# Kernel optimization log

Hardware: AMD Instinct MI355X
Metric: run time of the kernel (lower is better)

The kernel has to match this reference:

```python
import jax, jax.numpy as jnp
import numpy as np

B, N, F, P, HID, OUT = 4, 20000, 8, 12, 64, 1
E = 320000


def _glorot(k, shape):
    lim = float(np.sqrt(6.0 / (shape[0] + shape[1])))
    return jax.random.uniform(k, shape, jnp.float32, -lim, lim)


def setup_inputs() -> dict:
    key = jax.random.key(0)
    ks = jax.random.split(key, 20)
    inp = {
        "x": jax.random.normal(ks[0], (B, N, F, P), jnp.float32),
        "edge_index": jax.random.randint(ks[1], (2, E), 0, N, jnp.int64),
        "edge_attr": jax.random.uniform(ks[2], (E,), jnp.float32),
        # GCNConv weights (stored [in, out]) + biases for z, r, h gates
        "conv_z_w": _glorot(ks[3], (F, HID)), "conv_z_b": jnp.zeros((HID,), jnp.float32),
        "conv_r_w": _glorot(ks[4], (F, HID)), "conv_r_b": jnp.zeros((HID,), jnp.float32),
        "conv_h_w": _glorot(ks[5], (F, HID)), "conv_h_b": jnp.zeros((HID,), jnp.float32),
        # GRU linear layers on cat([conv_out, H]) -> HID (stored [in, out])
        "lin_z_w": _glorot(ks[6], (2 * HID, HID)), "lin_z_b": jnp.zeros((HID,), jnp.float32),
        "lin_r_w": _glorot(ks[7], (2 * HID, HID)), "lin_r_b": jnp.zeros((HID,), jnp.float32),
        "lin_h_w": _glorot(ks[8], (2 * HID, HID)), "lin_h_b": jnp.zeros((HID,), jnp.float32),
        # temporal attention logits over periods
        "attention": jax.random.uniform(ks[9], (P,), jnp.float32),
        # final linear: HID -> OUT*P
        "out_w": _glorot(ks[10], (HID, OUT * P)), "out_b": jnp.zeros((OUT * P,), jnp.float32),
    }
    return inp


def reference(x, edge_index, edge_attr,
              conv_z_w, conv_z_b, conv_r_w, conv_r_b, conv_h_w, conv_h_b,
              lin_z_w, lin_z_b, lin_r_w, lin_r_b, lin_h_w, lin_h_b,
              attention, out_w, out_b):
    Bb, Nn, Ff, Pp = x.shape
    Hh = conv_z_w.shape[1]

    # GCN normalization with self loops: A_hat = D^-1/2 (A + I) D^-1/2
    loop = jnp.arange(Nn)
    row = jnp.concatenate([edge_index[0], loop])
    col = jnp.concatenate([edge_index[1], loop])
    w = jnp.concatenate([edge_attr, jnp.ones((Nn,), x.dtype)])
    deg = jax.ops.segment_sum(w, col, num_segments=Nn)
    dinv = jnp.where(deg > 0, jax.lax.rsqrt(deg), 0.0)
    norm = dinv[row] * w * dinv[col]  # [E+N]

    def gcn(xt, W, b):
        # xt: [B, N, F] -> [B, N, H]
        xw = jnp.einsum('bnf,fh->bnh', xt, W)
        msg = xw[:, row, :] * norm[None, :, None]            # gather over source nodes
        agg = jax.vmap(lambda m: jax.ops.segment_sum(m, col, num_segments=Nn))(msg)
        return agg + b

    H0 = jnp.zeros((Bb, Nn, Hh), x.dtype)  # A3TGCN2 passes H=None each period -> zeros

    def tgcn_cell(xt):
        Z = jax.nn.sigmoid(jnp.concatenate([gcn(xt, conv_z_w, conv_z_b), H0], -1) @ lin_z_w + lin_z_b)
        R = jax.nn.sigmoid(jnp.concatenate([gcn(xt, conv_r_w, conv_r_b), H0], -1) @ lin_r_w + lin_r_b)
        Ht = jnp.tanh(jnp.concatenate([gcn(xt, conv_h_w, conv_h_b), H0 * R], -1) @ lin_h_w + lin_h_b)
        return Z * H0 + (1.0 - Z) * Ht

    probs = jax.nn.softmax(attention)
    xs = jnp.moveaxis(x, -1, 0)  # [P, B, N, F]

    def step(acc, inp):
        xt, p = inp
        return acc + p * tgcn_cell(xt), None

    h_accum, _ = jax.lax.scan(step, jnp.zeros((Bb, Nn, Hh), x.dtype), (xs, probs))

    h = jax.nn.relu(h_accum)
    out = h @ out_w + out_b                 # [B, N, OUT*P]
    return out.reshape(Bb, Nn, -1, Pp)      # [B, N, OUT, P]
```

## Files before the change

### kernel.cpp

```cpp
#include <hip/hip_runtime.h>

#define NN 20000
#define EE 320000
#define CAP 64
#define SVC 72
#define OVCAP 8192
#define EBLK 313

#define WZ_O 0
#define BZ_O 512
#define WH_O 576
#define BH_O 1088
#define OWT_O 1152
#define OB_O 1968
#define PR_O 1980
#define NCONST 1992

#define LOG2E 1.44269504088896340736f

__device__ __forceinline__ float b2f(unsigned short h) {
  union { unsigned int u; float f; } v; v.u = ((unsigned int)h) << 16; return v.f;
}
__device__ __forceinline__ unsigned short f2b(float f) {
  union { unsigned int u; float f; } v; v.f = f;
  unsigned int u = v.u;
  unsigned int r = (u + 0x7fffu + ((u >> 16) & 1u)) >> 16;
  return (unsigned short)r;
}
__device__ __forceinline__ float ldw(const void* p, int i, int isbf) {
  return isbf ? b2f(((const unsigned short*)p)[i]) : ((const float*)p)[i];
}
__device__ __forceinline__ void upk(unsigned int w, float& x0, float& x1) {
  union { unsigned int u; float f; } lo, hi;
  lo.u = w << 16; hi.u = w & 0xffff0000u;
  x0 = lo.f; x1 = hi.f;
}
__device__ __forceinline__ float degf(unsigned long long dc) {
  return (float)(unsigned int)dc * (1.0f / 1048576.0f);
}
__device__ __forceinline__ float ex2(float x) {
#if __has_builtin(__builtin_amdgcn_exp2f)
  return __builtin_amdgcn_exp2f(x);
#else
  return __exp2f(x);
#endif
}

struct __align__(4) U3 { unsigned int x, y, z; };

__global__ void __launch_bounds__(256) k_append(
    const void* __restrict__ ei, const void* __restrict__ ea,
    unsigned long long* __restrict__ degcnt,
    unsigned int* __restrict__ slab,
    int* __restrict__ ovf_cnt, int* __restrict__ ovf_dst,
    unsigned int* __restrict__ ovf_pack, float* __restrict__ consts,
    const void* czw, const void* czb, const void* chw, const void* chb,
    const void* lzw, const void* lzb, const void* lhw, const void* lhb,
    const void* att, const void* ow, const void* ob) {
  __shared__ int sfl[2];
  const int tid = threadIdx.x;
  if (tid < 64) {
    unsigned long long b1 = __ballot((((const unsigned int*)ea)[tid] >> 15) & 1u);
    unsigned long long b2 = __ballot(((const unsigned int*)ei)[2 * tid + 1] != 0u);
    if (tid == 0) {
      sfl[0] = (b1 == 0ull) ? 1 : 0;
      sfl[1] = (b2 == 0ull) ? 1 : 0;
    }
  }
  __syncthreads();
  const int isbf = sfl[0], is64 = sfl[1];

  if (blockIdx.x == EBLK) {
    for (int idx = tid; idx < 512; idx += 256) {
      int f = idx >> 6, k = idx & 63;
      float sz = 0.f, sh = 0.f;
      for (int h = 0; h < 64; ++h) {
        sz += ldw(czw, f * 64 + h, isbf) * ldw(lzw, h * 64 + k, isbf);
        sh += ldw(chw, f * 64 + h, isbf) * ldw(lhw, h * 64 + k, isbf);
      }
      consts[WZ_O + idx] = sz * LOG2E;
      consts[WH_O + idx] = sh * (2.0f * LOG2E);
    }
    for (int idx = tid; idx < 64; idx += 256) {
      float sz = ldw(lzb, idx, isbf), sh = ldw(lhb, idx, isbf);
      for (int h = 0; h < 64; ++h) {
        sz += ldw(czb, h, isbf) * ldw(lzw, h * 64 + idx, isbf);
        sh += ldw(chb, h, isbf) * ldw(lhw, h * 64 + idx, isbf);
      }
      consts[BZ_O + idx] = sz * LOG2E;
      consts[BH_O + idx] = sh * (2.0f * LOG2E);
    }
    for (int idx = tid; idx < 816; idx += 256) {
      int p = idx / 68, kk = idx % 68;
      consts[OWT_O + idx] = (kk < 64) ? ldw(ow, kk * 12 + p, isbf) : 0.f;
    }
    if (tid < 12) consts[OB_O + tid] = ldw(ob, tid, isbf);
    if (tid == 0) {
      float a[12]; float m = -1e30f;
      for (int p = 0; p < 12; ++p) { a[p] = ldw(att, p, isbf); m = fmaxf(m, a[p]); }
      float ssum = 0.f;
      for (int p = 0; p < 12; ++p) { a[p] = __expf(a[p] - m); ssum += a[p]; }
      for (int p = 0; p < 12; ++p) consts[PR_O + p] = a[p] / ssum;
    }
    return;
  }

  const int e0 = blockIdx.x * 1024 + tid;
#pragma unroll
  for (int u = 0; u < 4; ++u) {
    int e = e0 + 256 * u;
    if (e >= EE) continue;
    int r, c;
    if (is64) {
      r = (int)((const unsigned int*)ei)[2 * e];
      c = (int)((const unsigned int*)ei)[2 * (EE + e)];
    } else {
      r = ((const int*)ei)[e];
      c = ((const int*)ei)[EE + e];
    }
    unsigned short wb;
    float w;
    if (isbf) { wb = ((const unsigned short*)ea)[e]; w = b2f(wb); }
    else      { w = ((const float*)ea)[e]; wb = f2b(w); }
    unsigned long long pk = (1ull << 32) |
        (unsigned long long)(unsigned int)__float2int_rn(w * 1048576.0f);
    unsigned long long old = atomicAdd(&degcnt[c], pk);
    int pos = (int)(old >> 32);
    unsigned int packed = ((unsigned int)wb << 16) | (unsigned int)r;
    if (pos < CAP) {
      slab[c * CAP + pos] = packed;
    } else {
      int oi = atomicAdd(ovf_cnt, 1);
      if (oi < OVCAP) { ovf_dst[oi] = c; ovf_pack[oi] = packed; }
    }
  }
}

#define ACC6(u, v)                                           \
  { float x0, x1;                                            \
    upk((u).x, x0, x1); a[0] += (v) * x0; a[1] += (v) * x1;  \
    upk((u).y, x0, x1); a[2] += (v) * x0; a[3] += (v) * x1;  \
    upk((u).z, x0, x1); a[4] += (v) * x0; a[5] += (v) * x1; }

#define ACCF6(f0, f1, f2, v)                                                   \
  { a[0] += (v) * (f0).x; a[1] += (v) * (f0).y; a[2] += (v) * (f1).x;          \
    a[3] += (v) * (f1).y; a[4] += (v) * (f2).x; a[5] += (v) * (f2).y; }

__global__ void __launch_bounds__(256) k_node(
    const void* __restrict__ x, const void* __restrict__ ea,
    const unsigned long long* __restrict__ degcnt,
    const unsigned int* __restrict__ slab,
    const int* __restrict__ ovf_cnt, const int* __restrict__ ovf_dst,
    const unsigned int* __restrict__ ovf_pack,
    const float* __restrict__ consts,
    void* __restrict__ out) {
  __shared__ __align__(16) float sow[840];
  __shared__ __align__(16) int2  sv[4 * SVC];
  __shared__ __align__(16) float accT[4 * 384];
  __shared__ __align__(16) float hw[4 * 272];
  __shared__ int swcnt[4];
  __shared__ int sfl[1];

  const int tid  = threadIdx.x;
  const int w    = tid >> 6;
  const int lane = tid & 63;
  const int n    = blockIdx.x * 4 + w;

  if (tid < 64) {
    unsigned long long b1 = __ballot((((const unsigned int*)ea)[tid] >> 15) & 1u);
    if (tid == 0) sfl[0] = (b1 == 0ull) ? 1 : 0;
  }
  for (int i = tid; i < 840; i += 256) sow[i] = consts[OWT_O + i];
  float wz[8], wh[8];
#pragma unroll
  for (int f = 0; f < 8; ++f) {
    wz[f] = consts[WZ_O + f * 64 + lane];
    wh[f] = consts[WH_O + f * 64 + lane];
  }
  const float bz = consts[BZ_O + lane], bh = consts[BH_O + lane];
  __syncthreads();
  const int isbf = sfl[0];

  unsigned long long dcn = degcnt[n];
  int cnt = (int)(dcn >> 32);
  int base = cnt < CAP ? cnt : CAP;
  const float dn = rsqrtf(degf(dcn) + 1.0f);
  int2* svw = &sv[w * SVC];
  if (lane == 0) swcnt[w] = base;
  if (lane < base) {
    unsigned int pk = slab[n * CAP + lane];
    int s = (int)(pk & 0xffffu);
    float v = b2f((unsigned short)(pk >> 16)) * rsqrtf(degf(degcnt[s]) + 1.0f) * dn;
    svw[lane] = make_int2(s * 96, __float_as_int(v));
  }
  int m0 = base;
  {
    int ov = ovf_cnt[0];
    if (ov > 0) {
      if (ov > OVCAP) ov = OVCAP;
      for (int i = lane; i < ov; i += 64) {
        if (ovf_dst[i] == n) {
          int idx = atomicAdd(&swcnt[w], 1);
          if (idx < SVC - 1) {
            unsigned int pk = ovf_pack[i];
            int s = (int)(pk & 0xffffu);
            float v = b2f((unsigned short)(pk >> 16)) *
                      rsqrtf(degf(degcnt[s]) + 1.0f) * dn;
            svw[idx] = make_int2(s * 96, __float_as_int(v));
          }
        }
      }
      __builtin_amdgcn_wave_barrier();
      m0 = swcnt[w];
      if (m0 > SVC - 1) m0 = SVC - 1;
    }
  }
  if (lane == 0) svw[m0] = make_int2(n * 96, __float_as_int(dn * dn));
  const int m1 = m0 + 1;
  __builtin_amdgcn_wave_barrier();

  float a[6];
#pragma unroll
  for (int t = 0; t < 6; ++t) a[t] = 0.f;
  {
    const int i15 = lane & 15;
    const long xbase = (long)(lane >> 4) * (NN * 96) + 6 * i15;
    if (isbf) {
      const unsigned short* xr = (const unsigned short*)x + xbase;
      int j = 0;
      for (; j + 1 < m1; j += 2) {
        int2 e0 = svw[j], e1 = svw[j + 1];
        U3 u0 = *(const U3*)(xr + e0.x);
        U3 u1 = *(const U3*)(xr + e1.x);
        float v0 = __int_as_float(e0.y), v1 = __int_as_float(e1.y);
        ACC6(u0, v0); ACC6(u1, v1);
      }
      if (j < m1) {
        int2 e0 = svw[j];
        U3 u0 = *(const U3*)(xr + e0.x);
        float v0 = __int_as_float(e0.y);
        ACC6(u0, v0);
      }
    } else {
      const float* xf = (const float*)x + xbase;
      int j = 0;
      for (; j + 1 < m1; j += 2) {
        int2 e0 = svw[j], e1 = svw[j + 1];
        const float2* p0 = (const float2*)(xf + e0.x);
        const float2* p1 = (const float2*)(xf + e1.x);
        float2 u00 = p0[0], u01 = p0[1], u02 = p0[2];
        float2 u10 = p1[0], u11 = p1[1], u12 = p1[2];
        float v0 = __int_as_float(e0.y), v1 = __int_as_float(e1.y);
        ACCF6(u00, u01, u02, v0); ACCF6(u10, u11, u12, v1);
      }
      if (j < m1) {
        int2 e0 = svw[j];
        const float2* p0 = (const float2*)(xf + e0.x);
        float2 u00 = p0[0], u01 = p0[1], u02 = p0[2];
        float v0 = __int_as_float(e0.y);
        ACCF6(u00, u01, u02, v0);
      }
    }
    float* aw = &accT[w * 384 + (lane >> 4) * 96 + (i15 & 1) * 48 + (i15 >> 1)];
#pragma unroll
    for (int t = 0; t < 6; ++t) aw[8 * t] = a[t];
  }
  __builtin_amdgcn_wave_barrier();

  {
    const float* accTw = &accT[w * 384];
    float* hww = &hw[w * 272];
    float prv[12];
#pragma unroll
    for (int p = 0; p < 12; ++p) prv[p] = sow[828 + p];
#pragma unroll
    for (int b = 0; b < 4; ++b) {
      float hbl = 0.f;
#pragma unroll
      for (int p = 0; p < 12; ++p) {
        const float4* A = (const float4*)&accTw[b * 96 + p * 8];
        float4 A0 = A[0], A1 = A[1];
        float za = bz + A0.x * wz[0] + A0.y * wz[1] + A0.z * wz[2] + A0.w * wz[3]
                      + A1.x * wz[4] + A1.y * wz[5] + A1.z * wz[6] + A1.w * wz[7];
        float ta = bh + A0.x * wh[0] + A0.y * wh[1] + A0.z * wh[2] + A0.w * wh[3]
                      + A1.x * wh[4] + A1.y * wh[5] + A1.z * wh[6] + A1.w * wh[7];
        float ea2 = ex2(za);
        float eh = ex2(fminf(ta, 115.0f));
        float num = eh - 1.0f;
        float den = (1.0f + ea2) * (1.0f + eh);
        hbl += prv[p] * (num * __builtin_amdgcn_rcpf(den));
      }
      hww[b * 68 + lane] = fmaxf(hbl, 0.f);
    }
  }
  __builtin_amdgcn_wave_barrier();

  if (lane < 48) {
    const float* hww = &hw[w * 272];
    int b = lane / 12, p = lane % 12;
    float o = sow[816 + p];
#pragma unroll
    for (int kq = 0; kq < 16; ++kq) {
      float4 hv = *(const float4*)&hww[b * 68 + 4 * kq];
      float4 wv = *(const float4*)&sow[p * 68 + 4 * kq];
      o += hv.x * wv.x + hv.y * wv.y + hv.z * wv.z + hv.w * wv.w;
    }
    int oi = (b * NN + n) * 12 + p;
    if (isbf) ((unsigned short*)out)[oi] = f2b(o);
    else      ((float*)out)[oi] = o;
  }
}

extern "C" void kernel_launch(void* const* d_in, const int* in_sizes, int n_in,
                              void* d_out, int out_size, void* d_ws, size_t ws_size,
                              hipStream_t stream) {
  const void* x   = d_in[0];
  const void* ei  = d_in[1];
  const void* ea  = d_in[2];
  const void* czw = d_in[3];
  const void* czb = d_in[4];
  const void* chw = d_in[7];
  const void* chb = d_in[8];
  const void* lzw = d_in[9];
  const void* lzb = d_in[10];
  const void* lhw = d_in[13];
  const void* lhb = d_in[14];
  const void* att = d_in[15];
  const void* ow  = d_in[16];
  const void* ob  = d_in[17];

  char* ws = (char*)d_ws;
  float* consts  = (float*)(ws + 256);
  unsigned long long* degcnt = (unsigned long long*)(ws + 8448);
  int*   ovf_cnt = (int*)  (ws + 168448);
  int*   ovf_dst = (int*)  (ws + 168704);
  unsigned int* ovf_pack = (unsigned int*)(ws + 201472);
  unsigned int* slab     = (unsigned int*)(ws + 234240);

  hipMemsetAsync(ws + 8448, 0, 160064, stream);
  k_append<<<dim3(EBLK + 1), dim3(256), 0, stream>>>(ei, ea, degcnt, slab,
                                                     ovf_cnt, ovf_dst, ovf_pack,
                                                     consts,
                                                     czw, czb, chw, chb,
                                                     lzw, lzb, lhw, lhb,
                                                     att, ow, ob);
  k_node<<<dim3(NN / 4), dim3(256), 0, stream>>>(x, ea, degcnt, slab,
                                                 ovf_cnt, ovf_dst, ovf_pack,
                                                 consts, d_out);
}
```

Baseline: 230.8 us.

## Fuse edge append and node compute into one cooperative persistent kernel

Merges the edge-bucketing/constant-folding kernel and the per-node kernel into a single cooperative launch with a grid-wide sync between the phases. Phase two runs as persistent waves that pull nodes from an atomic work queue, and its inner accumulation uses packed FP32 FMA instructions. This is meant to remove the second launch and the gap between kernels and to balance per-node work. In exchange it adds grid-sync cost, a fixed grid of 1024 blocks with limited occupancy, and atomic contention on the queue counter, with a fallback to the old two-kernel path if the cooperative launch fails.

After: 230.0 us. About the same (-0.4%).

```diff
diff --git a/kernel.cpp b/kernel.cpp
--- a/kernel.cpp
+++ b/kernel.cpp
@@ -1,4 +1,7 @@
 #include <hip/hip_runtime.h>
+#include <hip/hip_cooperative_groups.h>
+
+namespace cg = cooperative_groups;
 
 #define NN 20000
 #define EE 320000
@@ -6,6 +9,8 @@
 #define SVC 72
 #define OVCAP 8192
 #define EBLK 313
+#define GRID 1024
+#define NWP 5
 
 #define WZ_O 0
 #define BZ_O 512
@@ -14,9 +19,22 @@
 #define OWT_O 1152
 #define OB_O 1968
 #define PR_O 1980
-#define NCONST 1992
 
 #define LOG2E 1.44269504088896340736f
+
+typedef float v2f __attribute__((ext_vector_type(2)));
+
+__device__ __forceinline__ v2f mk2(float a, float b) { v2f t; t.x = a; t.y = b; return t; }
+__device__ __forceinline__ v2f pkfma(v2f a, v2f b, v2f c) {
+  v2f d;
+  asm("v_pk_fma_f32 %0, %1, %2, %3" : "=v"(d) : "v"(a), "v"(b), "v"(c));
+  return d;
+}
+__device__ __forceinline__ v2f pkmul(v2f a, v2f b) {
+  v2f d;
+  asm("v_pk_mul_f32 %0, %1, %2" : "=v"(d) : "v"(a), "v"(b));
+  return d;
+}
 
 __device__ __forceinline__ float b2f(unsigned short h) {
   union { unsigned int u; float f; } v; v.u = ((unsigned int)h) << 16; return v.f;
@@ -45,8 +63,279 @@
   return __exp2f(x);
 #endif
 }
+__device__ __forceinline__ v2f bpk(unsigned int u) {
+  union { unsigned int i; float f; } lo, hi;
+  lo.i = u << 16; hi.i = u & 0xffff0000u;
+  return mk2(lo.f, hi.f);
+}
 
 struct __align__(4) U3 { unsigned int x, y, z; };
+
+#define ACC6P(u, vv)                              \
+  { aa0 = pkfma(bpk((u).x), vv, aa0);             \
+    aa1 = pkfma(bpk((u).y), vv, aa1);             \
+    aa2 = pkfma(bpk((u).z), vv, aa2); }
+
+__global__ void __launch_bounds__(256, 4) k_fused(
+    const void* __restrict__ x, const void* __restrict__ ei,
+    const void* __restrict__ ea,
+    const void* czw, const void* czb, const void* chw, const void* chb,
+    const void* lzw, const void* lzb, const void* lhw, const void* lhb,
+    const void* att, const void* ow, const void* ob,
+    unsigned long long* __restrict__ degcnt,
+    unsigned int* __restrict__ slab,
+    int* __restrict__ ovf_cnt, int* __restrict__ ovf_dst,
+    unsigned int* __restrict__ ovf_pack,
+    float* __restrict__ consts,
+    int* __restrict__ wq,
+    void* __restrict__ out) {
+  __shared__ __align__(16) float sow[840];
+  __shared__ __align__(16) int2  sv[4 * SVC];
+  __shared__ __align__(16) float accT[4 * 384];
+  __shared__ __align__(16) float hw[4 * 272];
+  __shared__ int swcnt[4];
+  __shared__ int sfl[2];
+
+  const int tid = threadIdx.x;
+  const int bid = blockIdx.x;
+  const int gsz = gridDim.x;
+
+  if (tid < 64) {
+    unsigned long long b1 = __ballot((((const unsigned int*)ea)[tid] >> 15) & 1u);
+    unsigned long long b2 = __ballot(((const unsigned int*)ei)[2 * tid + 1] != 0u);
+    if (tid == 0) {
+      sfl[0] = (b1 == 0ull) ? 1 : 0;
+      sfl[1] = (b2 == 0ull) ? 1 : 0;
+    }
+  }
+  __syncthreads();
+  const int isbf = sfl[0], is64 = sfl[1];
+
+  const int ebn = gsz - NWP;
+  if (bid < ebn) {
+    for (int e = bid * 256 + tid; e < EE; e += ebn * 256) {
+      int r, c;
+      if (is64) {
+        r = (int)((const unsigned int*)ei)[2 * e];
+        c = (int)((const unsigned int*)ei)[2 * (EE + e)];
+      } else {
+        r = ((const int*)ei)[e];
+        c = ((const int*)ei)[EE + e];
+      }
+      unsigned short wb;
+      float wv;
+      if (isbf) { wb = ((const unsigned short*)ea)[e]; wv = b2f(wb); }
+      else      { wv = ((const float*)ea)[e]; wb = f2b(wv); }
+      unsigned long long pk = (1ull << 32) |
+          (unsigned long long)(unsigned int)__float2int_rn(wv * 1048576.0f);
+      unsigned long long old = atomicAdd(&degcnt[c], pk);
+      int pos = (int)(old >> 32);
+      unsigned int packed = ((unsigned int)wb << 16) | (unsigned int)r;
+      if (pos < CAP) {
+        slab[c * CAP + pos] = packed;
+      } else {
+        int oi = atomicAdd(ovf_cnt, 1);
+        if (oi < OVCAP) { ovf_dst[oi] = c; ovf_pack[oi] = packed; }
+      }
+    }
+  } else {
+    int role = bid - ebn;
+    if (role < 4) {
+      for (int idx = role * 128 + tid; idx < (role + 1) * 128; idx += 256) {
+        int f = idx >> 6, k = idx & 63;
+        float sz = 0.f, sh = 0.f;
+        for (int h = 0; h < 64; ++h) {
+          sz += ldw(czw, f * 64 + h, isbf) * ldw(lzw, h * 64 + k, isbf);
+          sh += ldw(chw, f * 64 + h, isbf) * ldw(lhw, h * 64 + k, isbf);
+        }
+        consts[WZ_O + idx] = sz * LOG2E;
+        consts[WH_O + idx] = sh * (2.0f * LOG2E);
+      }
+    } else {
+      for (int idx = tid; idx < 64; idx += 256) {
+        float sz = ldw(lzb, idx, isbf), sh = ldw(lhb, idx, isbf);
+        for (int h = 0; h < 64; ++h) {
+          sz += ldw(czb, h, isbf) * ldw(lzw, h * 64 + idx, isbf);
+          sh += ldw(chb, h, isbf) * ldw(lhw, h * 64 + idx, isbf);
+        }
+        consts[BZ_O + idx] = sz * LOG2E;
+        consts[BH_O + idx] = sh * (2.0f * LOG2E);
+      }
+      for (int idx = tid; idx < 816; idx += 256) {
+        int p = idx / 68, kk = idx % 68;
+        consts[OWT_O + idx] = (kk < 64) ? ldw(ow, kk * 12 + p, isbf) : 0.f;
+      }
+      if (tid < 12) consts[OB_O + tid] = ldw(ob, tid, isbf);
+      if (tid == 0) {
+        float a[12]; float m = -1e30f;
+        for (int p = 0; p < 12; ++p) { a[p] = ldw(att, p, isbf); m = fmaxf(m, a[p]); }
+        float ssum = 0.f;
+        for (int p = 0; p < 12; ++p) { a[p] = __expf(a[p] - m); ssum += a[p]; }
+        for (int p = 0; p < 12; ++p) consts[PR_O + p] = a[p] / ssum;
+      }
+    }
+  }
+
+  cg::this_grid().sync();
+
+  const int w    = tid >> 6;
+  const int lane = tid & 63;
+
+  for (int i = tid; i < 840; i += 256) sow[i] = consts[OWT_O + i];
+  v2f wzp[4], whp[4];
+#pragma unroll
+  for (int j = 0; j < 4; ++j) {
+    wzp[j] = mk2(consts[WZ_O + (2 * j) * 64 + lane], consts[WZ_O + (2 * j + 1) * 64 + lane]);
+    whp[j] = mk2(consts[WH_O + (2 * j) * 64 + lane], consts[WH_O + (2 * j + 1) * 64 + lane]);
+  }
+  const float bz = consts[BZ_O + lane], bh = consts[BH_O + lane];
+  float prv[12];
+#pragma unroll
+  for (int p = 0; p < 12; ++p) prv[p] = consts[PR_O + p];
+  __syncthreads();
+
+  int ovt = ovf_cnt[0];
+  if (ovt > OVCAP) ovt = OVCAP;
+
+  for (;;) {
+    int n;
+    if (lane == 0) n = atomicAdd(wq, 1);
+    n = __shfl(n, 0);
+    if (n >= NN) break;
+
+    unsigned long long dcn = degcnt[n];
+    int cnt = (int)(dcn >> 32);
+    int base = cnt < CAP ? cnt : CAP;
+    const float dn = rsqrtf(degf(dcn) + 1.0f);
+    int2* svw = &sv[w * SVC];
+    if (lane == 0) swcnt[w] = base;
+    if (lane < base) {
+      unsigned int pk = slab[n * CAP + lane];
+      int s = (int)(pk & 0xffffu);
+      float v = b2f((unsigned short)(pk >> 16)) * rsqrtf(degf(degcnt[s]) + 1.0f) * dn;
+      svw[lane] = make_int2(s * 96, __float_as_int(v));
+    }
+    int m0 = base;
+    if (ovt > 0) {
+      for (int i = lane; i < ovt; i += 64) {
+        if (ovf_dst[i] == n) {
+          int idx = atomicAdd(&swcnt[w], 1);
+          if (idx < SVC - 1) {
+            unsigned int pk = ovf_pack[i];
+            int s = (int)(pk & 0xffffu);
+            float v = b2f((unsigned short)(pk >> 16)) *
+                      rsqrtf(degf(degcnt[s]) + 1.0f) * dn;
+            svw[idx] = make_int2(s * 96, __float_as_int(v));
+          }
+        }
+      }
+      __builtin_amdgcn_wave_barrier();
+      m0 = swcnt[w];
+      if (m0 > SVC - 1) m0 = SVC - 1;
+    }
+    if (lane == 0) svw[m0] = make_int2(n * 96, __float_as_int(dn * dn));
+    const int m1 = m0 + 1;
+    __builtin_amdgcn_wave_barrier();
+
+    v2f aa0 = mk2(0.f, 0.f), aa1 = mk2(0.f, 0.f), aa2 = mk2(0.f, 0.f);
+    const int i15 = lane & 15;
+    const long xbase = (long)(lane >> 4) * (NN * 96) + 6 * i15;
+    if (isbf) {
+      const unsigned short* xr = (const unsigned short*)x + xbase;
+      int j = 0;
+      for (; j + 1 < m1; j += 2) {
+        int2 e0 = svw[j], e1 = svw[j + 1];
+        U3 u0 = *(const U3*)(xr + e0.x);
+        U3 u1 = *(const U3*)(xr + e1.x);
+        v2f vv0 = mk2(__int_as_float(e0.y), __int_as_float(e0.y));
+        v2f vv1 = mk2(__int_as_float(e1.y), __int_as_float(e1.y));
+        ACC6P(u0, vv0); ACC6P(u1, vv1);
+      }
+      if (j < m1) {
+        int2 e0 = svw[j];
+        U3 u0 = *(const U3*)(xr + e0.x);
+        v2f vv0 = mk2(__int_as_float(e0.y), __int_as_float(e0.y));
+        ACC6P(u0, vv0);
+      }
+    } else {
+      const float* xf = (const float*)x + xbase;
+      int j = 0;
+      for (; j + 1 < m1; j += 2) {
+        int2 e0 = svw[j], e1 = svw[j + 1];
+        const v2f* p0 = (const v2f*)(xf + e0.x);
+        const v2f* p1 = (const v2f*)(xf + e1.x);
+        v2f u00 = p0[0], u01 = p0[1], u02 = p0[2];
+        v2f u10 = p1[0], u11 = p1[1], u12 = p1[2];
+        v2f vv0 = mk2(__int_as_float(e0.y), __int_as_float(e0.y));
+        v2f vv1 = mk2(__int_as_float(e1.y), __int_as_float(e1.y));
+        aa0 = pkfma(u00, vv0, aa0); aa1 = pkfma(u01, vv0, aa1); aa2 = pkfma(u02, vv0, aa2);
+        aa0 = pkfma(u10, vv1, aa0); aa1 = pkfma(u11, vv1, aa1); aa2 = pkfma(u12, vv1, aa2);
+      }
+      if (j < m1) {
+        int2 e0 = svw[j];
+        const v2f* p0 = (const v2f*)(xf + e0.x);
+        v2f vv0 = mk2(__int_as_float(e0.y), __int_as_float(e0.y));
+        aa0 = pkfma(p0[0], vv0, aa0); aa1 = pkfma(p0[1], vv0, aa1); aa2 = pkfma(p0[2], vv0, aa2);
+      }
+    }
+    {
+      float* aw = &accT[w * 384 + (lane >> 4) * 96 + (i15 & 1) * 48 + (i15 >> 1)];
+      aw[0]  = aa0.x; aw[8]  = aa0.y;
+      aw[16] = aa1.x; aw[24] = aa1.y;
+      aw[32] = aa2.x; aw[40] = aa2.y;
+    }
+    __builtin_amdgcn_wave_barrier();
+
+    {
+      const float* accTw = &accT[w * 384];
+      float* hww = &hw[w * 272];
+#pragma unroll
+      for (int b = 0; b < 4; ++b) {
+        float hbl = 0.f;
+#pragma unroll
+        for (int p = 0; p < 12; ++p) {
+          const float4* A = (const float4*)&accTw[b * 96 + p * 8];
+          float4 A0 = A[0], A1 = A[1];
+          v2f zv = pkmul(mk2(A0.x, A0.y), wzp[0]);
+          zv = pkfma(mk2(A0.z, A0.w), wzp[1], zv);
+          zv = pkfma(mk2(A1.x, A1.y), wzp[2], zv);
+          zv = pkfma(mk2(A1.z, A1.w), wzp[3], zv);
+          v2f tv = pkmul(mk2(A0.x, A0.y), whp[0]);
+          tv = pkfma(mk2(A0.z, A0.w), whp[1], tv);
+          tv = pkfma(mk2(A1.x, A1.y), whp[2], tv);
+          tv = pkfma(mk2(A1.z, A1.w), whp[3], tv);
+          float za = zv.x + zv.y + bz;
+          float ta = tv.x + tv.y + bh;
+          float ea2 = ex2(za);
+          float eh = ex2(fminf(ta, 115.0f));
+          float num = eh - 1.0f;
+          float den = (1.0f + ea2) * (1.0f + eh);
+          hbl += prv[p] * (num * __builtin_amdgcn_rcpf(den));
+        }
+        hww[b * 68 + lane] = fmaxf(hbl, 0.f);
+      }
+    }
+    __builtin_amdgcn_wave_barrier();
+
+    if (lane < 48) {
+      const float* hww = &hw[w * 272];
+      int b = lane / 12, p = lane % 12;
+      v2f acc2 = mk2(0.f, 0.f);
+#pragma unroll
+      for (int kq = 0; kq < 16; ++kq) {
+        float4 hv = *(const float4*)&hww[b * 68 + 4 * kq];
+        float4 wv = *(const float4*)&sow[p * 68 + 4 * kq];
+        acc2 = pkfma(mk2(hv.x, hv.y), mk2(wv.x, wv.y), acc2);
+        acc2 = pkfma(mk2(hv.z, hv.w), mk2(wv.z, wv.w), acc2);
+      }
+      float o = acc2.x + acc2.y + sow[816 + p];
+      int oi = (b * NN + n) * 12 + p;
+      if (isbf) ((unsigned short*)out)[oi] = f2b(o);
+      else      ((float*)out)[oi] = o;
+    }
+    __builtin_amdgcn_wave_barrier();
+  }
+}
 
 __global__ void __launch_bounds__(256) k_append(
     const void* __restrict__ ei, const void* __restrict__ ea,
@@ -333,11 +622,30 @@
   float* consts  = (float*)(ws + 256);
   unsigned long long* degcnt = (unsigned long long*)(ws + 8448);
   int*   ovf_cnt = (int*)  (ws + 168448);
+  int*   wq      = (int*)  (ws + 168512);
   int*   ovf_dst = (int*)  (ws + 168704);
   unsigned int* ovf_pack = (unsigned int*)(ws + 201472);
   unsigned int* slab     = (unsigned int*)(ws + 234240);
 
-  hipMemsetAsync(ws + 8448, 0, 160064, stream);
+  hipMemsetAsync(ws + 8448, 0, 160128, stream);
+
+  static int mode = 0;
+  if (mode == 0) {
+    void* outp = d_out;
+    void* args[22] = {
+        (void*)&x,  (void*)&ei,  (void*)&ea,
+        (void*)&czw, (void*)&czb, (void*)&chw, (void*)&chb,
+        (void*)&lzw, (void*)&lzb, (void*)&lhw, (void*)&lhb,
+        (void*)&att, (void*)&ow,  (void*)&ob,
+        (void*)&degcnt, (void*)&slab, (void*)&ovf_cnt, (void*)&ovf_dst,
+        (void*)&ovf_pack, (void*)&consts, (void*)&wq, (void*)&outp};
+    hipError_t err = hipLaunchCooperativeKernel(k_fused, dim3(GRID), dim3(256),
+                                                args, 0u, stream);
+    if (err == hipSuccess) return;
+    (void)hipGetLastError();
+    mode = 1;
+  }
+
   k_append<<<dim3(EBLK + 1), dim3(256), 0, stream>>>(ei, ea, degcnt, slab,
                                                      ovf_cnt, ovf_dst, ovf_pack,
                                                      consts,
```
